# Performance work log

Measured on AMD Instinct MI355X. Metric: run time of the kernel, lower is better.

## Reference

```python
import jax, jax.numpy as jnp
import numpy as np

CX, CY, FX, FY = 334.081, 169.808, 460.585, 460.268
EPS = 1e-07
T_ITER = 1000
MIN_POINTS = 5000
H, W, B = 360, 640, 2


def _point_cloud(depth_img):
    # depth_img: [C,H,W]; channel 2 if C==3 else channel 0
    depth = depth_img[2] if depth_img.shape[0] == 3 else depth_img[0]
    rows, cols = depth.shape
    c = jnp.arange(cols, dtype=depth.dtype)[None, :]
    r = jnp.arange(rows, dtype=depth.dtype)[:, None]
    valid = (depth > 0) & (depth < 65535)
    nanv = jnp.float32(jnp.nan)
    z = jnp.where(valid, depth / 1000.0, nanv)
    x = jnp.where(valid, z * (c - CX) / FX, nanv)
    y = jnp.where(valid, z * (r - CY) / FY, nanv)
    pcd = jnp.stack([x.ravel(), y.ravel(), z.ravel()], axis=1)  # [N,3]
    return pcd, valid.ravel()


def setup_inputs() -> dict:
    key = jax.random.key(0)
    k1, k2 = jax.random.split(key)
    fake = jax.random.uniform(k1, (B, 1, H, W), dtype=jnp.float32)
    real = jax.random.uniform(k2, (B, 1, H, W), dtype=jnp.float32)
    return {"fake": fake, "real": real, "epoch": 5, "show_image": 0}


def _forward(fake, real, epoch):
    real_pcd, vr = _point_cloud(real[0])
    fake_pcd, vf = _point_cloud(fake[0])
    real_pcd = real_pcd * 1000.0
    fake_pcd = fake_pcd * 1000.0
    # pcd[pcd==0] = eps  (NaN==0 is False, NaNs preserved)
    real_pcd = jnp.where(real_pcd == 0, EPS, real_pcd)
    fake_pcd = jnp.where(fake_pcd == 0, EPS, fake_pcd)

    # combined validity mask (real-valid then fake-valid filtering chain)
    m = vr & vf
    cnt = jnp.maximum(jnp.sum(m), 1)

    def sel(v, fill):
        return jnp.where(m, v, fill)

    def mrmse(a, b):
        d = sel(a, 0.0) - sel(b, 0.0)
        return jnp.sqrt(jnp.sum(d * d) / cnt)

    lossX = mrmse(real_pcd[:, 0], fake_pcd[:, 0])
    lossY = mrmse(real_pcd[:, 1], fake_pcd[:, 1])
    lossZ = mrmse(real_pcd[:, 2], fake_pcd[:, 2])
    dlog = jnp.log(jnp.abs(sel(real_pcd[:, 2], 1.0))) - jnp.log(jnp.abs(sel(fake_pcd[:, 2], 1.0)))
    RMSE_log = 10000.0 * jnp.sqrt(jnp.sum(jnp.where(m, dlog * dlog, 0.0)) / cnt)
    loss17 = RMSE_log * jnp.abs(10.0 * (3.0 - jnp.exp(lossX) - jnp.exp(lossY) - jnp.exp(lossZ)))

    # ---- batched RANSAC plane fit on normalized fake cloud ----
    nan_cloud = jnp.where(jnp.isnan(fake_pcd), 0.0, fake_pcd)
    pts = nan_cloud / jnp.max(nan_cloud)  # [N,3]
    N = pts.shape[0]
    thresh = jnp.maximum(jnp.float32(0.025 - 0.001 * epoch), jnp.float32(0.005))

    rkey = jax.random.key(42)
    idx = jax.random.randint(rkey, (T_ITER, 3), 0, N)  # 3 sample points per trial
    p = pts[idx]  # [T,3,3]
    vA = p[:, 1] - p[:, 0]
    vB = p[:, 2] - p[:, 0]
    nrm = jnp.cross(vA, vB)
    nrm = nrm / jnp.linalg.norm(nrm, axis=1, keepdims=True)  # unit normals [T,3]
    kk = -jnp.sum(nrm * p[:, 1], axis=1)  # plane offsets [T]
    dist = pts @ nrm.T + kk[None, :]  # [N,T], |n|=1 so no extra divide
    inl = jnp.abs(dist) <= thresh  # [N,T]
    counts = jnp.sum(inl, axis=0)  # [T]
    # keep first trial with strictly-largest count among counts > minPoints
    score = jnp.where(counts > MIN_POINTS, counts, -1)
    best = jnp.argmax(score)
    a, b, c, d = nrm[best, 0], nrm[best, 1], nrm[best, 2], kk[best]
    inlier_mask = inl[:, best]  # [N]

    # translation/rotation were built via torch.tensor(...) -> detached in torch
    trans = jax.lax.stop_gradient(jnp.stack([jnp.zeros(()), jnp.zeros(()), d / c]))
    n2 = a * a + b * b + c * c
    cos_t = c / jnp.sqrt(n2)
    sin_t = jnp.sqrt((a * a + b * b) / n2)
    sab = jnp.sqrt(a * a + b * b)
    u1 = b / sab
    u2 = -a / sab
    R = jnp.stack([
        jnp.stack([cos_t + u1 * u1 * (1 - cos_t), u1 * u2 * (1 - cos_t), u2 * sin_t]),
        jnp.stack([u1 * u2 * (1 - cos_t), cos_t + u2 * u2 * (1 - cos_t), -u1 * sin_t]),
        jnp.stack([-u2 * sin_t, u1 * sin_t, cos_t]),
    ])
    Rt = jax.lax.stop_gradient(R).T  # torch transposes before matmul

    plane_pts = pts + trans
    zc = (plane_pts @ Rt)[:, 2]  # rotated z for all points; inliers selected by mask
    icnt = jnp.maximum(jnp.sum(inlier_mask), 1)
    zmax = jnp.max(jnp.where(inlier_mask, zc, -jnp.inf))
    zmin = jnp.min(jnp.where(inlier_mask, zc, jnp.inf))
    below = jnp.sum(jnp.where(inlier_mask, jnp.abs(zc - zmax), 0.0)) / icnt
    above = jnp.sum(jnp.where(inlier_mask, jnp.abs(zc - zmin), 0.0)) / icnt
    above = jnp.where(above == 0, jnp.float32(1e-07), above)
    plane_mean_dist_grad = 1000.0 * (above + below)

    loss_curv = loss17 + plane_mean_dist_grad
    delta = jnp.stack([RMSE_log, lossX, lossY, lossZ, plane_mean_dist_grad, loss17])
    return delta, loss_curv


def reference(fake, real, epoch, show_image):
    del show_image  # unused in the loss math
    return _forward(fake, real, epoch)
```

## Files before the change

### kernel.cpp

```cpp
#include <hip/hip_runtime.h>

namespace {

typedef float v2f __attribute__((ext_vector_type(2)));

constexpr int kW = 640;
constexpr unsigned kSpan = 230400u;
constexpr int kB1 = 900;
constexpr int kB3 = 1024;
constexpr int kPPB3 = 225;
constexpr int kB5 = 900;

constexpr size_t kOffMaxv    = 0;
constexpr size_t kOffL17     = 8;
constexpr size_t kOffSel     = 16;
constexpr size_t kOffPlanes  = 512;
constexpr size_t kOffSP      = 512 + 16384;
constexpr size_t kOffZP      = 61440;
constexpr size_t kOffPartial = 98304;
constexpr size_t kOffPts     = 2097152;

__device__ __forceinline__ unsigned rotl32(unsigned v, int r) {
  return (v << r) | (v >> (32 - r));
}

__device__ __forceinline__ void threefry(unsigned c0, unsigned c1,
                                         unsigned& o0, unsigned& o1) {
  const unsigned ks0 = 0u, ks1 = 42u, ks2 = 0x1BD11BDAu ^ 0u ^ 42u;
  unsigned x0 = c0 + ks0, x1 = c1 + ks1;
#define TFR(r) { x0 += x1; x1 = rotl32(x1, (r)); x1 ^= x0; }
  TFR(13) TFR(15) TFR(26) TFR(6)
  x0 += ks1; x1 += ks2 + 1u;
  TFR(17) TFR(29) TFR(16) TFR(24)
  x0 += ks2; x1 += ks0 + 2u;
  TFR(13) TFR(15) TFR(26) TFR(6)
  x0 += ks0; x1 += ks1 + 3u;
  TFR(17) TFR(29) TFR(16) TFR(24)
  x0 += ks1; x1 += ks2 + 4u;
  TFR(13) TFR(15) TFR(26) TFR(6)
  x0 += ks2; x1 += ks0 + 5u;
#undef TFR
  o0 = x0; o1 = x1;
}

__device__ __forceinline__ void pix_coords(float d, int row, int col, bool& valid,
                                           float& x, float& y, float& z) {
  valid = (d > 0.0f) && (d < 65535.0f);
  float z0 = d / 1000.0f;
  float x0 = z0 * ((float)col - 334.081f) / 460.585f;
  float y0 = z0 * ((float)row - 169.808f) / 460.268f;
  x = x0 * 1000.0f;
  y = y0 * 1000.0f;
  z = z0 * 1000.0f;
  if (x == 0.0f) x = 1e-7f;
  if (y == 0.0f) y = 1e-7f;
  if (z == 0.0f) z = 1e-7f;
}

__device__ __forceinline__ void make_pt(float d, int row, int col, float maxv,
                                        float& x, float& y, float& z) {
  bool v; float a, b, c;
  pix_coords(d, row, col, v, a, b, c);
  x = (v ? a : 0.f) / maxv;
  y = (v ? b : 0.f) / maxv;
  z = (v ? c : 0.f) / maxv;
}

__device__ __forceinline__ float get_thresh(int ep) {
  return (float)fmax(0.025 - 0.001 * (double)ep, 0.005);
}

__global__ __launch_bounds__(256) void k_stats(const float* __restrict__ fake,
                                               const float* __restrict__ real,
                                               char* __restrict__ ws) {
  int* maxvBits = (int*)(ws + kOffMaxv);
  double* sp = (double*)(ws + kOffSP);
  float4* ptsraw = (float4*)(ws + kOffPts);

  const int b = blockIdx.x, t = threadIdx.x;
  const int lane = t & 63, wid = t >> 6;

  __shared__ double sD0[4], sD1[4], sD2[4], sD3[4];
  __shared__ int sI0[4];
  __shared__ float sF0[4];

  int i = b * 256 + t;
  int row = i / kW, col = i - row * kW;
  bool vr, vf; float rx, ry, rz, fx, fy, fz;
  pix_coords(real[i], row, col, vr, rx, ry, rz);
  pix_coords(fake[i], row, col, vf, fx, fy, fz);
  ptsraw[i] = make_float4(vf ? fx : 0.f, vf ? fy : 0.f, vf ? fz : 0.f, 0.f);
  double dx2 = 0, dy2 = 0, dz2 = 0, dl2 = 0; int cc = 0;
  if (vr && vf) {
    float ddx = rx - fx, ddy = ry - fy, ddz = rz - fz;
    dx2 = (double)ddx * (double)ddx;
    dy2 = (double)ddy * (double)ddy;
    dz2 = (double)ddz * (double)ddz;
    double dl = log(fabs((double)rz)) - log(fabs((double)fz));
    dl2 = dl * dl;
    cc = 1;
  }
  float mx = vf ? fmaxf(fmaxf(fx, fy), fz) : 0.0f;
  for (int o = 32; o; o >>= 1) {
    dx2 += __shfl_down(dx2, o); dy2 += __shfl_down(dy2, o);
    dz2 += __shfl_down(dz2, o); dl2 += __shfl_down(dl2, o);
    cc += __shfl_down(cc, o);
    mx = fmaxf(mx, __shfl_down(mx, o));
  }
  if (lane == 0) { sD0[wid]=dx2; sD1[wid]=dy2; sD2[wid]=dz2; sD3[wid]=dl2;
                   sI0[wid]=cc; sF0[wid]=mx; }
  __syncthreads();
  if (t == 0) {
    double* e = sp + (size_t)b * 6;
    e[0] = sD0[0]+sD0[1]+sD0[2]+sD0[3];
    e[1] = sD1[0]+sD1[1]+sD1[2]+sD1[3];
    e[2] = sD2[0]+sD2[1]+sD2[2]+sD2[3];
    e[3] = sD3[0]+sD3[1]+sD3[2]+sD3[3];
    e[4] = (double)(sI0[0]+sI0[1]+sI0[2]+sI0[3]);
    float bm = fmaxf(fmaxf(sF0[0], sF0[1]), fmaxf(sF0[2], sF0[3]));
    atomicMax(maxvBits, (int)__float_as_uint(bm));
  }
}

__global__ __launch_bounds__(256) void k_mid(const float* __restrict__ fake,
                                             float* __restrict__ out,
                                             char* __restrict__ ws) {
  const int* maxvBits = (const int*)(ws + kOffMaxv);
  double* loss17p = (double*)(ws + kOffL17);
  unsigned* selkeyp = (unsigned*)(ws + kOffSel);
  float4* planes = (float4*)(ws + kOffPlanes);
  const double* sp = (const double*)(ws + kOffSP);
  float4* pts = (float4*)(ws + kOffPts);

  const int t = threadIdx.x;
  const int lane = t & 63, wid = t >> 6;

  if (blockIdx.x >= 17) {
    const float maxv = __uint_as_float((unsigned)*maxvBits);
    int i = (blockIdx.x - 17) * 256 + t;
    float4 r = pts[i];
    pts[i] = make_float4(r.x / maxv, r.y / maxv, r.z / maxv, 0.f);
  } else if (blockIdx.x == 16) {
    __shared__ double sD0[4], sD1[4], sD2[4], sD3[4];
    __shared__ int sI0[4];
    double gx = 0, gy = 0, gz = 0, gl = 0; int gc = 0;
    for (int r = t; r < kB1; r += 256) {
      const double* e = sp + (size_t)r * 6;
      gx += e[0]; gy += e[1]; gz += e[2]; gl += e[3];
      gc += (int)e[4];
    }
    for (int o = 32; o; o >>= 1) {
      gx += __shfl_down(gx, o); gy += __shfl_down(gy, o);
      gz += __shfl_down(gz, o); gl += __shfl_down(gl, o);
      gc += __shfl_down(gc, o);
    }
    if (lane == 0) { sD0[wid]=gx; sD1[wid]=gy; sD2[wid]=gz; sD3[wid]=gl; sI0[wid]=gc; }
    __syncthreads();
    if (t == 0) {
      double SX = sD0[0]+sD0[1]+sD0[2]+sD0[3];
      double SY = sD1[0]+sD1[1]+sD1[2]+sD1[3];
      double SZ = sD2[0]+sD2[1]+sD2[2]+sD2[3];
      double SL = sD3[0]+sD3[1]+sD3[2]+sD3[3];
      int CN = sI0[0]+sI0[1]+sI0[2]+sI0[3];
      double cntd = (CN > 0) ? (double)CN : 1.0;
      double lossX = sqrt(SX / cntd);
      double lossY = sqrt(SY / cntd);
      double lossZ = sqrt(SZ / cntd);
      double rmse_log = 10000.0 * sqrt(SL / cntd);
      double loss17 = rmse_log * fabs(10.0 * (3.0 - exp(lossX) - exp(lossY) - exp(lossZ)));
      *loss17p = loss17;
      *selkeyp = 0u;
      out[0] = (float)rmse_log;
      out[1] = (float)lossX;
      out[2] = (float)lossY;
      out[3] = (float)lossZ;
      out[5] = (float)loss17;
    }
  } else {
    const float maxv = __uint_as_float((unsigned)*maxvBits);
    __shared__ float sX[192], sY[192], sZ[192];
    if (t < 192) {
      int j = t / 3;
      int v = t - j * 3;
      int pid = blockIdx.x * 64 + j;
      if (pid < 1000) {
        unsigned p = 3u * (unsigned)pid + (unsigned)v;
        unsigned o0, o1;
        threefry(p, p + 3000u, o0, o1);
        unsigned idx = o1 % kSpan;
        int row = (int)(idx / kW), col = (int)idx - row * kW;
        float x, y, z;
        make_pt(fake[idx], row, col, maxv, x, y, z);
        sX[t] = x; sY[t] = y; sZ[t] = z;
      }
    }
    __syncthreads();
    if (t < 64) {
      int pid = blockIdx.x * 64 + t;
      if (pid < 1000) {
        float px[3], py[3], pz[3];
#pragma unroll
        for (int v = 0; v < 3; v++) {
          px[v] = sX[3 * t + v]; py[v] = sY[3 * t + v]; pz[v] = sZ[3 * t + v];
        }
        float ax = px[1]-px[0], ay = py[1]-py[0], az = pz[1]-pz[0];
        float bx = px[2]-px[0], by = py[2]-py[0], bz = pz[2]-pz[0];
        float nx = ay*bz - az*by;
        float ny = az*bx - ax*bz;
        float nz = ax*by - ay*bx;
        float nn = sqrtf(nx*nx + ny*ny + nz*nz);
        nx /= nn; ny /= nn; nz /= nn;
        float kk = -(nx*px[1] + ny*py[1] + nz*pz[1]);
        planes[pid] = make_float4(nx, ny, nz, kk);
      } else {
        planes[pid] = make_float4(0.f, 0.f, 0.f, 3e38f);
      }
    }
  }
}

__global__ __launch_bounds__(256) void k_count(const int* __restrict__ epoch,
                                               const float4* __restrict__ planes,
                                               const float4* __restrict__ pts,
                                               unsigned* __restrict__ partial) {
  const int b = blockIdx.x, t = threadIdx.x;
  const float th = get_thresh(*epoch);

  float4 p0 = planes[t * 4 + 0], p1 = planes[t * 4 + 1];
  float4 p2 = planes[t * 4 + 2], p3 = planes[t * 4 + 3];
  v2f Ax = {p0.x, p1.x}, Ay = {p0.y, p1.y}, Az = {p0.z, p1.z}, Aw = {p0.w, p1.w};
  v2f Bx = {p2.x, p3.x}, By = {p2.y, p3.y}, Bz = {p2.z, p3.z}, Bw = {p2.w, p3.w};

  const float4* __restrict__ base = pts + b * kPPB3;

  int c0 = 0, c1 = 0, c2 = 0, c3 = 0;
#pragma unroll 5
  for (int s = 0; s < kPPB3; ++s) {
    float4 q = base[s];
    v2f qx = {q.x, q.x}, qy = {q.y, q.y}, qz = {q.z, q.z};
    v2f dA = __builtin_elementwise_fma(qx, Ax,
             __builtin_elementwise_fma(qy, Ay,
             __builtin_elementwise_fma(qz, Az, Aw)));
    v2f dB = __builtin_elementwise_fma(qx, Bx,
             __builtin_elementwise_fma(qy, By,
             __builtin_elementwise_fma(qz, Bz, Bw)));
    c0 += (fabsf(dA.x) <= th) ? 1 : 0;
    c1 += (fabsf(dA.y) <= th) ? 1 : 0;
    c2 += (fabsf(dB.x) <= th) ? 1 : 0;
    c3 += (fabsf(dB.y) <= th) ? 1 : 0;
  }
  partial[b * 256 + t] =
      (unsigned)c0 | ((unsigned)c1 << 8) | ((unsigned)c2 << 16) | ((unsigned)c3 << 24);
}

__global__ __launch_bounds__(256) void k_select(char* __restrict__ ws) {
  unsigned* selkeyp = (unsigned*)(ws + kOffSel);
  const unsigned* partial = (const unsigned*)(ws + kOffPartial);

  const int r = blockIdx.x;
  const int t = threadIdx.x;

  __shared__ uint4 sAcc[16][16];

  int owner = r * 16 + (t & 15);
  int chunk = t >> 4;
  unsigned s0 = 0, s1 = 0, s2 = 0, s3 = 0;
  for (int row = chunk * 64; row < chunk * 64 + 64; ++row) {
    unsigned v = partial[row * 256 + owner];
    s0 += v & 0xFFu; s1 += (v >> 8) & 0xFFu;
    s2 += (v >> 16) & 0xFFu; s3 += (v >> 24) & 0xFFu;
  }
  sAcc[t & 15][chunk] = make_uint4(s0, s1, s2, s3);
  __syncthreads();

  unsigned mykey = 0u;
  if (t < 16) {
    unsigned t0 = 0, t1 = 0, t2 = 0, t3 = 0;
    for (int j = 0; j < 16; ++j) {
      uint4 v = sAcc[t][j];
      t0 += v.x; t1 += v.y; t2 += v.z; t3 += v.w;
    }
    unsigned tot[4] = {t0, t1, t2, t3};
    int pbase = (r * 16 + t) * 4;
#pragma unroll
    for (int k = 0; k < 4; ++k) {
      int p = pbase + k;
      if (p < 1000) {
        int score = ((int)tot[k] > 5000) ? (int)tot[k] : -1;
        unsigned key = ((unsigned)(score + 2) << 10) | (unsigned)(1023 - p);
        mykey = key > mykey ? key : mykey;
      }
    }
  }
  for (int o = 32; o; o >>= 1) {
    unsigned other = __shfl_down(mykey, o);
    mykey = other > mykey ? other : mykey;
  }
  if (t == 0) atomicMax(selkeyp, mykey);
}

__global__ __launch_bounds__(256) void k_zc(const int* __restrict__ epoch,
                                            char* __restrict__ ws) {
  const float4* planes = (const float4*)(ws + kOffPlanes);
  unsigned long long* zp = (unsigned long long*)(ws + kOffZP);
  const float4* pts = (const float4*)(ws + kOffPts);

  const int b = blockIdx.x, t = threadIdx.x;
  const int lane = t & 63, wid = t >> 6;
  const float th = get_thresh(*epoch);

  unsigned selkey = *(const unsigned*)(ws + kOffSel);
  int best = 1023 - (int)(selkey & 1023u);
  float4 pl = planes[best];
  const float a = pl.x, bb = pl.y, c = pl.z, d = pl.w;
  float n2 = a * a + bb * bb + c * c;
  float cos_t = c / sqrtf(n2);
  float sin_t = sqrtf((a * a + bb * bb) / n2);
  float sab = sqrtf(a * a + bb * bb);
  float u1 = bb / sab, u2 = -a / sab;
  const float r0 = -u2 * sin_t, r1 = u1 * sin_t, r2 = cos_t, tz = d / c;

  __shared__ double sD0[4];
  __shared__ int sI0[4];
  __shared__ float sF0[4], sF1[4];

  double sz = 0.0; int ic = 0; float zmx = -INFINITY, zmn = -INFINITY;
  {
    float4 q = pts[b * 256 + t];
    float dist = fmaf(q.x, a, fmaf(q.y, bb, fmaf(q.z, c, d)));
    if (fabsf(dist) <= th) {
      float zc = fmaf(q.x, r0, fmaf(q.y, r1, (q.z + tz) * r2));
      sz = (double)zc; ic = 1; zmx = zc; zmn = -zc;
    }
  }
  for (int o = 32; o; o >>= 1) {
    sz += __shfl_down(sz, o); ic += __shfl_down(ic, o);
    zmx = fmaxf(zmx, __shfl_down(zmx, o));
    zmn = fmaxf(zmn, __shfl_down(zmn, o));
  }
  if (lane == 0) { sD0[wid] = sz; sI0[wid] = ic; sF0[wid] = zmx; sF1[wid] = zmn; }
  __syncthreads();
  if (t == 0) {
    unsigned long long* e = zp + (size_t)b * 4;
    e[0] = __double_as_longlong(sD0[0]+sD0[1]+sD0[2]+sD0[3]);
    e[1] = (unsigned long long)(sI0[0]+sI0[1]+sI0[2]+sI0[3]);
    float bmx = fmaxf(fmaxf(sF0[0], sF0[1]), fmaxf(sF0[2], sF0[3]));
    float bmn = fmaxf(fmaxf(sF1[0], sF1[1]), fmaxf(sF1[2], sF1[3]));
    e[2] = (unsigned long long)__float_as_uint(bmx) |
           ((unsigned long long)__float_as_uint(bmn) << 32);
  }
}

__global__ __launch_bounds__(256) void k_final(float* __restrict__ out,
                                               char* __restrict__ ws) {
  const double* loss17p = (const double*)(ws + kOffL17);
  const unsigned long long* zp = (const unsigned long long*)(ws + kOffZP);

  const int t = threadIdx.x;
  const int lane = t & 63, wid = t >> 6;

  __shared__ double sD0[4];
  __shared__ int sI0[4];
  __shared__ float sF0[4], sF1[4];

  double gs = 0.0; int gi = 0; float gmx = -INFINITY, gmn = -INFINITY;
  for (int r = t; r < kB5; r += 256) {
    const unsigned long long* e = zp + (size_t)r * 4;
    gs += __longlong_as_double(e[0]);
    gi += (int)e[1];
    unsigned long long mm = e[2];
    gmx = fmaxf(gmx, __uint_as_float((unsigned)(mm & 0xFFFFFFFFu)));
    gmn = fmaxf(gmn, __uint_as_float((unsigned)(mm >> 32)));
  }
  for (int o = 32; o; o >>= 1) {
    gs += __shfl_down(gs, o); gi += __shfl_down(gi, o);
    gmx = fmaxf(gmx, __shfl_down(gmx, o));
    gmn = fmaxf(gmn, __shfl_down(gmn, o));
  }
  if (lane == 0) { sD0[wid] = gs; sI0[wid] = gi; sF0[wid] = gmx; sF1[wid] = gmn; }
  __syncthreads();
  if (t == 0) {
    double S = sD0[0]+sD0[1]+sD0[2]+sD0[3];
    int IC = sI0[0]+sI0[1]+sI0[2]+sI0[3];
    float MX = fmaxf(fmaxf(sF0[0], sF0[1]), fmaxf(sF0[2], sF0[3]));
    float MN = fmaxf(fmaxf(sF1[0], sF1[1]), fmaxf(sF1[2], sF1[3]));
    double below = 0.0, above = 0.0;
    if (IC > 0) {
      double icd = (double)IC;
      double mean = S / icd;
      below = (double)MX - mean;
      above = mean - (double)(-MN);
    }
    if (above == 0.0) above = 1e-7;
    double pmdg = 1000.0 * (above + below);
    out[4] = (float)pmdg;
    out[6] = (float)(*loss17p + pmdg);
  }
}

}

extern "C" void kernel_launch(void* const* d_in, const int* in_sizes, int n_in,
                              void* d_out, int out_size, void* d_ws, size_t ws_size,
                              hipStream_t stream) {
  (void)in_sizes; (void)n_in; (void)out_size; (void)ws_size;
  const float* fake = (const float*)d_in[0];
  const float* real = (const float*)d_in[1];
  const int* epoch = (const int*)d_in[2];
  float* out = (float*)d_out;
  char* ws = (char*)d_ws;

  const float4* planes = (const float4*)(ws + kOffPlanes);
  const float4* pts    = (const float4*)(ws + kOffPts);
  unsigned* partial    = (unsigned*)(ws + kOffPartial);

  k_stats<<<kB1, 256, 0, stream>>>(fake, real, ws);
  k_mid<<<917, 256, 0, stream>>>(fake, out, ws);
  k_count<<<kB3, 256, 0, stream>>>(epoch, planes, pts, partial);
  k_select<<<16, 256, 0, stream>>>(ws);
  k_zc<<<kB5, 256, 0, stream>>>(epoch, ws);
  k_final<<<1, 256, 0, stream>>>(out, ws);
}
```

Baseline: 125.4 us.

## Split plane inlier counting across two blocks per point chunk

The inlier-count kernel now launches twice as many blocks, each thread evaluating two planes instead of four, with the plane set split in halves by block parity. Partial counts are packed as two 16-bit fields, and the selection kernel is reworked to gather the new layout, summing per plane across four chunks in shared memory. The partial buffer moves to a new workspace offset because it doubled in size. This trades more point loads and a larger partial buffer for more parallelism and lower per-thread register pressure.

```diff
diff --git a/kernel.cpp b/kernel.cpp
--- a/kernel.cpp
+++ b/kernel.cpp
@@ -7,7 +7,7 @@
 constexpr int kW = 640;
 constexpr unsigned kSpan = 230400u;
 constexpr int kB1 = 900;
-constexpr int kB3 = 1024;
+constexpr int kB3 = 2048;
 constexpr int kPPB3 = 225;
 constexpr int kB5 = 900;
 
@@ -17,8 +17,8 @@
 constexpr size_t kOffPlanes  = 512;
 constexpr size_t kOffSP      = 512 + 16384;
 constexpr size_t kOffZP      = 61440;
-constexpr size_t kOffPartial = 98304;
 constexpr size_t kOffPts     = 2097152;
+constexpr size_t kOffPartial = 6291456;
 
 __device__ __forceinline__ unsigned rotl32(unsigned v, int r) {
   return (v << r) | (v >> (32 - r));
@@ -224,16 +224,16 @@
                                                const float4* __restrict__ pts,
                                                unsigned* __restrict__ partial) {
   const int b = blockIdx.x, t = threadIdx.x;
+  const int pb = b >> 1, ph = b & 1;
   const float th = get_thresh(*epoch);
 
-  float4 p0 = planes[t * 4 + 0], p1 = planes[t * 4 + 1];
-  float4 p2 = planes[t * 4 + 2], p3 = planes[t * 4 + 3];
+  int pid = ph * 512 + t * 2;
+  float4 p0 = planes[pid + 0], p1 = planes[pid + 1];
   v2f Ax = {p0.x, p1.x}, Ay = {p0.y, p1.y}, Az = {p0.z, p1.z}, Aw = {p0.w, p1.w};
-  v2f Bx = {p2.x, p3.x}, By = {p2.y, p3.y}, Bz = {p2.z, p3.z}, Bw = {p2.w, p3.w};
-
-  const float4* __restrict__ base = pts + b * kPPB3;
-
-  int c0 = 0, c1 = 0, c2 = 0, c3 = 0;
+
+  const float4* __restrict__ base = pts + pb * kPPB3;
+
+  int c0 = 0, c1 = 0;
 #pragma unroll 5
   for (int s = 0; s < kPPB3; ++s) {
     float4 q = base[s];
@@ -241,16 +241,10 @@
     v2f dA = __builtin_elementwise_fma(qx, Ax,
              __builtin_elementwise_fma(qy, Ay,
              __builtin_elementwise_fma(qz, Az, Aw)));
-    v2f dB = __builtin_elementwise_fma(qx, Bx,
-             __builtin_elementwise_fma(qy, By,
-             __builtin_elementwise_fma(qz, Bz, Bw)));
     c0 += (fabsf(dA.x) <= th) ? 1 : 0;
     c1 += (fabsf(dA.y) <= th) ? 1 : 0;
-    c2 += (fabsf(dB.x) <= th) ? 1 : 0;
-    c3 += (fabsf(dB.y) <= th) ? 1 : 0;
-  }
-  partial[b * 256 + t] =
-      (unsigned)c0 | ((unsigned)c1 << 8) | ((unsigned)c2 << 16) | ((unsigned)c3 << 24);
+  }
+  partial[b * 256 + t] = (unsigned)c0 | ((unsigned)c1 << 16);
 }
 
 __global__ __launch_bounds__(256) void k_select(char* __restrict__ ws) {
@@ -260,36 +254,29 @@
   const int r = blockIdx.x;
   const int t = threadIdx.x;
 
-  __shared__ uint4 sAcc[16][16];
-
-  int owner = r * 16 + (t & 15);
-  int chunk = t >> 4;
-  unsigned s0 = 0, s1 = 0, s2 = 0, s3 = 0;
-  for (int row = chunk * 64; row < chunk * 64 + 64; ++row) {
-    unsigned v = partial[row * 256 + owner];
-    s0 += v & 0xFFu; s1 += (v >> 8) & 0xFFu;
-    s2 += (v >> 16) & 0xFFu; s3 += (v >> 24) & 0xFFu;
-  }
-  sAcc[t & 15][chunk] = make_uint4(s0, s1, s2, s3);
+  __shared__ unsigned sAcc[64][5];
+
+  int l = t & 63;
+  int chunk = t >> 6;
+  int p = r * 64 + l;
+  int ph = p >> 9;
+  int to = (p & 511) >> 1;
+  int j = p & 1;
+  unsigned cnt = 0;
+  for (int pb = chunk * 256; pb < chunk * 256 + 256; ++pb) {
+    unsigned v = partial[(pb * 2 + ph) * 256 + to];
+    cnt += (v >> (16 * j)) & 0xFFFFu;
+  }
+  sAcc[l][chunk] = cnt;
   __syncthreads();
 
   unsigned mykey = 0u;
-  if (t < 16) {
-    unsigned t0 = 0, t1 = 0, t2 = 0, t3 = 0;
-    for (int j = 0; j < 16; ++j) {
-      uint4 v = sAcc[t][j];
-      t0 += v.x; t1 += v.y; t2 += v.z; t3 += v.w;
-    }
-    unsigned tot[4] = {t0, t1, t2, t3};
-    int pbase = (r * 16 + t) * 4;
-#pragma unroll
-    for (int k = 0; k < 4; ++k) {
-      int p = pbase + k;
-      if (p < 1000) {
-        int score = ((int)tot[k] > 5000) ? (int)tot[k] : -1;
-        unsigned key = ((unsigned)(score + 2) << 10) | (unsigned)(1023 - p);
-        mykey = key > mykey ? key : mykey;
-      }
+  if (t < 64) {
+    unsigned tot = sAcc[t][0] + sAcc[t][1] + sAcc[t][2] + sAcc[t][3];
+    int p2 = r * 64 + t;
+    if (p2 < 1000) {
+      int score = ((int)tot > 5000) ? (int)tot : -1;
+      mykey = ((unsigned)(score + 2) << 10) | (unsigned)(1023 - p2);
     }
   }
   for (int o = 32; o; o >>= 1) {
```

Measured after the change: 135.9 us. +8.4%, slower.
